# Performance work log

Hardware: AMD Instinct MI355X
Metric: run time of the kernel (lower is better)

The kernel has to match this reference:

```python
import jax, jax.numpy as jnp
import numpy as np

S, B, D, H = 197, 64, 768, 12
E, K = 8, 2
LM, LS = 2, 2
DFF = 4 * D


def layer_norm(x, s, b):
    x32 = x.astype(jnp.float32)
    mu = x32.mean(-1, keepdims=True)
    var = x32.var(-1, keepdims=True)
    y = (x32 - mu) * jax.lax.rsqrt(var + 1e-5) * s + b
    return y.astype(x.dtype)


def quick_gelu(x):
    return x * jax.nn.sigmoid(1.702 * x)


def mha(x, in_w, in_b, out_w, out_b):
    # x: [S, B, D]; torch nn.MultiheadAttention math
    s, b, d = x.shape
    hd = d // H
    qkv = x @ in_w.T + in_b  # [S, B, 3D]
    q, k, v = jnp.split(qkv, 3, axis=-1)
    def heads(t):
        return t.reshape(s, b, H, hd).transpose(1, 2, 0, 3)  # [B, H, S, hd]
    q, k, v = heads(q), heads(k), heads(v)
    scale = 1.0 / np.sqrt(hd).astype(np.float32)
    scores = jnp.einsum('bhqd,bhkd->bhqk', q * scale, k)
    attn = jax.nn.softmax(scores, axis=-1)
    o = jnp.einsum('bhqk,bhkd->bhqd', attn, v)
    o = o.transpose(2, 0, 1, 3).reshape(s, b, d)
    return o @ out_w.T + out_b


def route(flat, gate_w):
    logits = flat @ gate_w.T  # [T, E]
    probs = jax.nn.softmax(logits.astype(jnp.float32), axis=-1)
    w, idx = jax.lax.top_k(probs, K)  # [T, K]
    w = w / w.sum(-1, keepdims=True)
    w = w.astype(flat.dtype)
    # combine weights [T, E]: routing weight where expert selected, else 0
    comb = (jax.nn.one_hot(idx, E, dtype=w.dtype) * w[..., None]).sum(axis=1)
    return logits, comb


def moe_ffn(flat, comb, w1, b1, w2, b2):
    # w1: [E, DFF, D], w2: [E, D, DFF]; exact top-k math via zero combine weights
    out = jnp.zeros_like(flat)
    for e in range(E):
        h = quick_gelu(flat @ w1[e].T + b1[e])
        out = out + comb[:, e:e + 1] * (h @ w2[e].T + b2[e])
    return out


def forward(x,
            moe_ln1_s, moe_ln1_b, moe_in_w, moe_in_b, moe_out_w, moe_out_b,
            moe_ln2_s, moe_ln2_b, moe_gate_w, moe_w1, moe_b1, moe_w2, moe_b2,
            std_ln1_s, std_ln1_b, std_in_w, std_in_b, std_out_w, std_out_b,
            std_ln2_s, std_ln2_b, std_fc_w, std_fc_b, std_proj_w, std_proj_b):
    first_logits = None
    comb = None
    for i in range(LM):
        h = x + mha(layer_norm(x, moe_ln1_s[i], moe_ln1_b[i]),
                    moe_in_w[i], moe_in_b[i], moe_out_w[i], moe_out_b[i])
        hs = layer_norm(h, moe_ln2_s[i], moe_ln2_b[i])
        flat = hs.reshape(-1, D)  # [S*B, D]
        if i == 0:
            first_logits, comb = route(flat, moe_gate_w[0])
        # subsequent MoE blocks reuse the first block's routing decision
        out_flat = moe_ffn(flat, comb, moe_w1[i], moe_b1[i], moe_w2[i], moe_b2[i])
        x = h + out_flat.reshape(h.shape)
    for i in range(LS):
        x = x + mha(layer_norm(x, std_ln1_s[i], std_ln1_b[i]),
                    std_in_w[i], std_in_b[i], std_out_w[i], std_out_b[i])
        y = layer_norm(x, std_ln2_s[i], std_ln2_b[i])
        y = quick_gelu(y @ std_fc_w[i].T + std_fc_b[i])
        x = x + (y @ std_proj_w[i].T + std_proj_b[i])
    return x, first_logits


def setup_inputs() -> dict:
    key = jax.random.key(0)
    ks = jax.random.split(key, 16)
    def n(k, shape, s=0.02):
        return jax.random.normal(k, shape, jnp.float32) * s
    inp = {}
    inp['x'] = jax.random.normal(ks[0], (S, B, D), jnp.float32)
    inp['moe_ln1_s'] = jnp.ones((LM, D), jnp.float32)
    inp['moe_ln1_b'] = jnp.zeros((LM, D), jnp.float32)
    inp['moe_in_w'] = n(ks[1], (LM, 3 * D, D))
    inp['moe_in_b'] = jnp.zeros((LM, 3 * D), jnp.float32)
    inp['moe_out_w'] = n(ks[2], (LM, D, D))
    inp['moe_out_b'] = jnp.zeros((LM, D), jnp.float32)
    inp['moe_ln2_s'] = jnp.ones((LM, D), jnp.float32)
    inp['moe_ln2_b'] = jnp.zeros((LM, D), jnp.float32)
    inp['moe_gate_w'] = n(ks[3], (LM, E, D))
    inp['moe_w1'] = n(ks[4], (LM, E, DFF, D))
    inp['moe_b1'] = jnp.zeros((LM, E, DFF), jnp.float32)
    inp['moe_w2'] = n(ks[5], (LM, E, D, DFF))
    inp['moe_b2'] = jnp.zeros((LM, E, D), jnp.float32)
    inp['std_ln1_s'] = jnp.ones((LS, D), jnp.float32)
    inp['std_ln1_b'] = jnp.zeros((LS, D), jnp.float32)
    inp['std_in_w'] = n(ks[6], (LS, 3 * D, D))
    inp['std_in_b'] = jnp.zeros((LS, 3 * D), jnp.float32)
    inp['std_out_w'] = n(ks[7], (LS, D, D))
    inp['std_out_b'] = jnp.zeros((LS, D), jnp.float32)
    inp['std_ln2_s'] = jnp.ones((LS, D), jnp.float32)
    inp['std_ln2_b'] = jnp.zeros((LS, D), jnp.float32)
    inp['std_fc_w'] = n(ks[8], (LS, DFF, D))
    inp['std_fc_b'] = jnp.zeros((LS, DFF), jnp.float32)
    inp['std_proj_w'] = n(ks[9], (LS, D, DFF))
    inp['std_proj_b'] = jnp.zeros((LS, D), jnp.float32)
    return inp


def reference(x,
              moe_ln1_s, moe_ln1_b, moe_in_w, moe_in_b, moe_out_w, moe_out_b,
              moe_ln2_s, moe_ln2_b, moe_gate_w, moe_w1, moe_b1, moe_w2, moe_b2,
              std_ln1_s, std_ln1_b, std_in_w, std_in_b, std_out_w, std_out_b,
              std_ln2_s, std_ln2_b, std_fc_w, std_fc_b, std_proj_w, std_proj_b):
    return forward(x,
                   moe_ln1_s, moe_ln1_b, moe_in_w, moe_in_b, moe_out_w, moe_out_b,
                   moe_ln2_s, moe_ln2_b, moe_gate_w, moe_w1, moe_b1, moe_w2, moe_b2,
                   std_ln1_s, std_ln1_b, std_in_w, std_in_b, std_out_w, std_out_b,
                   std_ln2_s, std_ln2_b, std_fc_w, std_fc_b, std_proj_w, std_proj_b)
```

## Files before the change

### kernel.cpp

```cpp
#include <hip/hip_runtime.h>

#define TOK   12608
#define SLOTS 25216
#define DM    768
#define D3    2304
#define FF    3072
#define NH    12
#define SEQ   197
#define BAT   64
#define NE    8
#define VPAD  224

typedef short  short8  __attribute__((ext_vector_type(8)));
typedef float  floatx4 __attribute__((ext_vector_type(4)));

__device__ __forceinline__ unsigned short f2bf(float f) {
  union { float f; unsigned u; } c; c.f = f;
  unsigned r = c.u + 0x7fffu + ((c.u >> 16) & 1u);
  return (unsigned short)(r >> 16);
}
__device__ __forceinline__ float bf2f(unsigned short h) {
  union { unsigned u; float f; } c; c.u = ((unsigned)h) << 16; return c.f;
}

__device__ __forceinline__ void gl2lds16(const void* g, void* l) {
  __builtin_amdgcn_global_load_lds((const __attribute__((address_space(1))) unsigned int*)g,
                                   (__attribute__((address_space(3))) unsigned int*)l, 16, 0, 0);
}


__global__ __launch_bounds__(256) void copy_k(float* __restrict__ dst, const float* __restrict__ src, long long n4) {
  long long i = (long long)blockIdx.x * 256 + threadIdx.x;
  long long st = (long long)gridDim.x * 256;
  for (; i < n4; i += st) ((floatx4*)dst)[i] = ((const floatx4*)src)[i];
}

__global__ __launch_bounds__(256) void conv_k(unsigned short* __restrict__ dst, const float* __restrict__ src, long long n4) {
  long long i = (long long)blockIdx.x * 256 + threadIdx.x;
  long long st = (long long)gridDim.x * 256;
  for (; i < n4; i += st) {
    floatx4 v = ((const floatx4*)src)[i];
    union { unsigned short u[4]; unsigned long long ll; } o;
    o.u[0] = f2bf(v.x); o.u[1] = f2bf(v.y); o.u[2] = f2bf(v.z); o.u[3] = f2bf(v.w);
    ((unsigned long long*)dst)[i] = o.ll;
  }
}

__global__ __launch_bounds__(256) void conv2_k(unsigned short* __restrict__ dhi, unsigned short* __restrict__ dlo,
                                               const float* __restrict__ src, long long n4) {
  long long i = (long long)blockIdx.x * 256 + threadIdx.x;
  long long st = (long long)gridDim.x * 256;
  for (; i < n4; i += st) {
    floatx4 v = ((const floatx4*)src)[i];
    union { unsigned short u[4]; unsigned long long ll; } oh, ol;
    #pragma unroll
    for (int j = 0; j < 4; ++j) {
      unsigned short h = f2bf(v[j]);
      oh.u[j] = h; ol.u[j] = f2bf(v[j] - bf2f(h));
    }
    ((unsigned long long*)dhi)[i] = oh.ll;
    ((unsigned long long*)dlo)[i] = ol.ll;
  }
}

__global__ void zero_k(int* p, int n) { int i = threadIdx.x; if (i < n) p[i] = 0; }

__global__ __launch_bounds__(256) void ln_k(const float* __restrict__ x, const float* __restrict__ s,
                                            const float* __restrict__ b, unsigned short* __restrict__ out) {
  int t = blockIdx.x * 4 + (threadIdx.x >> 6);
  int lane = threadIdx.x & 63;
  const float* xr = x + (long long)t * DM;
  float v[12]; float s1 = 0.f, s2 = 0.f;
  #pragma unroll
  for (int i = 0; i < 12; ++i) { v[i] = xr[lane + i*64]; s1 += v[i]; s2 += v[i]*v[i]; }
  #pragma unroll
  for (int o = 1; o < 64; o <<= 1) { s1 += __shfl_xor(s1, o); s2 += __shfl_xor(s2, o); }
  float mu = s1 * (1.f/768.f);
  float inv = 1.f / sqrtf(s2*(1.f/768.f) - mu*mu + 1e-5f);
  unsigned short* orow = out + (long long)t * DM;
  #pragma unroll
  for (int i = 0; i < 12; ++i) { int f = lane + i*64; orow[f] = f2bf((v[i]-mu)*inv*s[f] + b[f]); }
}

__global__ __launch_bounds__(256) void ln2bf_k(const float* __restrict__ x, const float* __restrict__ s,
                                               const float* __restrict__ b, unsigned short* __restrict__ ohi,
                                               unsigned short* __restrict__ olo) {
  int t = blockIdx.x * 4 + (threadIdx.x >> 6);
  int lane = threadIdx.x & 63;
  const float* xr = x + (long long)t * DM;
  float v[12]; float s1 = 0.f, s2 = 0.f;
  #pragma unroll
  for (int i = 0; i < 12; ++i) { v[i] = xr[lane + i*64]; s1 += v[i]; s2 += v[i]*v[i]; }
  #pragma unroll
  for (int o = 1; o < 64; o <<= 1) { s1 += __shfl_xor(s1, o); s2 += __shfl_xor(s2, o); }
  float mu = s1 * (1.f/768.f);
  float inv = 1.f / sqrtf(s2*(1.f/768.f) - mu*mu + 1e-5f);
  unsigned short* rh = ohi + (long long)t * DM;
  unsigned short* rl = olo + (long long)t * DM;
  #pragma unroll
  for (int i = 0; i < 12; ++i) {
    int f = lane + i*64;
    float y = (v[i]-mu)*inv*s[f] + b[f];
    unsigned short h = f2bf(y);
    rh[f] = h; rl[f] = f2bf(y - bf2f(h));
  }
}

__global__ __launch_bounds__(256) void gate_k(const float* __restrict__ x, const float* __restrict__ s,
    const float* __restrict__ b, const float* __restrict__ gw, float* __restrict__ logitsOut,
    int* __restrict__ e0, int* __restrict__ e1, float* __restrict__ w0, float* __restrict__ w1) {
  int t = blockIdx.x * 4 + (threadIdx.x >> 6);
  int lane = threadIdx.x & 63;
  const float* xr = x + (long long)t * DM;
  float v[12]; float s1 = 0.f, s2 = 0.f;
  #pragma unroll
  for (int i = 0; i < 12; ++i) { v[i] = xr[lane + i*64]; s1 += v[i]; s2 += v[i]*v[i]; }
  #pragma unroll
  for (int o = 1; o < 64; o <<= 1) { s1 += __shfl_xor(s1, o); s2 += __shfl_xor(s2, o); }
  float mu = s1 * (1.f/768.f);
  float inv = 1.f / sqrtf(s2*(1.f/768.f) - mu*mu + 1e-5f);
  float lg[8];
  #pragma unroll
  for (int e = 0; e < 8; ++e) lg[e] = 0.f;
  #pragma unroll
  for (int i = 0; i < 12; ++i) {
    int f = lane + i*64;
    float y = (v[i]-mu)*inv*s[f] + b[f];
    #pragma unroll
    for (int e = 0; e < 8; ++e) lg[e] += y * gw[e*DM + f];
  }
  #pragma unroll
  for (int e = 0; e < 8; ++e) {
    #pragma unroll
    for (int o = 1; o < 64; o <<= 1) lg[e] += __shfl_xor(lg[e], o);
  }
  if (lane == 0) {
    int a0 = 0;
    #pragma unroll
    for (int e = 1; e < 8; ++e) if (lg[e] > lg[a0]) a0 = e;
    int a1 = (a0 == 0) ? 1 : 0;
    #pragma unroll
    for (int e = 0; e < 8; ++e) if (e != a0 && lg[e] > lg[a1]) a1 = e;
    float mx = lg[a0];
    float pa = __expf(lg[a0]-mx), pb = __expf(lg[a1]-mx), iw = 1.f/(pa+pb);
    e0[t] = a0; e1[t] = a1; w0[t] = pa*iw; w1[t] = pb*iw;
    #pragma unroll
    for (int e = 0; e < 8; ++e) logitsOut[(long long)t*8 + e] = lg[e];
  }
}

__global__ __launch_bounds__(256) void hist_k(const int* __restrict__ e0, const int* __restrict__ e1,
                                              int* __restrict__ counts) {
  __shared__ int hc[8];
  int tid = threadIdx.x;
  if (tid < 8) hc[tid] = 0;
  __syncthreads();
  int c[8];
  #pragma unroll
  for (int e = 0; e < 8; ++e) c[e] = 0;
  for (int t = blockIdx.x * 256 + tid; t < TOK; t += gridDim.x * 256) {
    int a = e0[t], b = e1[t];
    #pragma unroll
    for (int e = 0; e < 8; ++e) c[e] += (a == e) + (b == e);
  }
  #pragma unroll
  for (int e = 0; e < 8; ++e) {
    #pragma unroll
    for (int o = 1; o < 64; o <<= 1) c[e] += __shfl_xor(c[e], o);
  }
  if ((tid & 63) == 0) {
    #pragma unroll
    for (int e = 0; e < 8; ++e) atomicAdd(&hc[e], c[e]);
  }
  __syncthreads();
  if (tid < 8 && hc[tid]) atomicAdd(&counts[tid], hc[tid]);
}

__global__ void tilemap_k(const int* __restrict__ counts, int* __restrict__ cur,
                          int4* __restrict__ tileMap, int* __restrict__ tileCount) {
  if (threadIdx.x == 0 && blockIdx.x == 0) {
    int off = 0, nt = 0;
    for (int e = 0; e < 8; ++e) {
      cur[e] = off;
      int cnt = counts[e];
      for (int s = 0; s < cnt; s += 128) {
        int rows = cnt - s; if (rows > 128) rows = 128;
        tileMap[nt++] = make_int4(e, off + s, rows, 0);
      }
      off += cnt;
    }
    *tileCount = nt;
  }
}

__global__ __launch_bounds__(256) void scatter_k(const int* __restrict__ e0, const int* __restrict__ e1,
    const float* __restrict__ w0, const float* __restrict__ w1, int* __restrict__ cur,
    int* __restrict__ perm, float* __restrict__ wslot, int* __restrict__ slotA, int* __restrict__ slotB) {
  int t = blockIdx.x * 256 + threadIdx.x;
  int lane = threadIdx.x & 63;
  bool valid = t < TOK;
  int a = valid ? e0[t] : -1;
  int b = valid ? e1[t] : -1;
  int sa = 0, sb = 0;
  #pragma unroll
  for (int e = 0; e < 8; ++e) {
    unsigned long long m = __ballot(a == e);
    int cnt = (int)__popcll(m);
    int base = 0;
    if (lane == 0 && cnt) base = atomicAdd(&cur[e], cnt);
    base = __shfl(base, 0);
    if (a == e) sa = base + (int)__popcll(m & ((1ull << lane) - 1ull));

    unsigned long long m2 = __ballot(b == e);
    int cnt2 = (int)__popcll(m2);
    int base2 = 0;
    if (lane == 0 && cnt2) base2 = atomicAdd(&cur[e], cnt2);
    base2 = __shfl(base2, 0);
    if (b == e) sb = base2 + (int)__popcll(m2 & ((1ull << lane) - 1ull));
  }
  if (valid) {
    perm[sa] = t; wslot[sa] = w0[t]; slotA[t] = sa;
    perm[sb] = t; wslot[sb] = w1[t]; slotB[t] = sb;
  }
}

__global__ __launch_bounds__(256) void combine_k(float* __restrict__ x, const float* __restrict__ Y,
    const int* __restrict__ sA, const int* __restrict__ sB) {
  int idx = blockIdx.x * 256 + threadIdx.x;
  int t = idx / (DM/4), f = idx % (DM/4);
  const floatx4* ya = (const floatx4*)(Y + (long long)sA[t]*DM);
  const floatx4* yb = (const floatx4*)(Y + (long long)sB[t]*DM);
  floatx4* xp = (floatx4*)(x + (long long)t*DM);
  xp[f] = xp[f] + ya[f] + yb[f];
}

__global__ __launch_bounds__(256) void vtrans_k(const unsigned short* __restrict__ hi,
    const unsigned short* __restrict__ lo, unsigned short* __restrict__ vThi,
    unsigned short* __restrict__ vTlo) {
  __shared__ unsigned short tH[64][65], tL[64][65];
  int bh = blockIdx.x; int b = bh / NH, h = bh % NH;
  int t = threadIdx.x; int d = t & 63, sl = t >> 6;
  for (int chunk = 0; chunk < 4; ++chunk) {
    __syncthreads();
    #pragma unroll
    for (int r = 0; r < 16; ++r) {
      int sp = r*4 + sl;
      int sg = chunk*64 + sp;
      unsigned short vh = 0, vl = 0;
      if (sg < SEQ) {
        long long off = (long long)(sg*BAT + b)*D3 + 2*DM + h*64 + d;
        vh = hi[off]; vl = lo[off];
      }
      tH[sp][d] = vh; tL[sp][d] = vl;
    }
    __syncthreads();
    int s2 = t & 63, dd0 = t >> 6;
    if (chunk*64 + s2 < VPAD) {
      #pragma unroll
      for (int r = 0; r < 16; ++r) {
        int dd = r*4 + dd0;
        long long oi = ((long long)bh*64 + dd)*VPAD + chunk*64 + s2;
        vThi[oi] = tH[s2][dd];
        vTlo[oi] = tL[s2][dd];
      }
    }
  }
}

template<int MODE, bool GATHER, bool PERM>
__global__ __launch_bounds__(256) void gemm_k(
    const unsigned short* __restrict__ A, const unsigned short* __restrict__ Bw,
    const float* __restrict__ bias, int M, int N, int K,
    const int* __restrict__ perm, const int4* __restrict__ tileMap,
    const int* __restrict__ tileCount, const float* __restrict__ wslot,
    unsigned short* __restrict__ outB, float* __restrict__ outF,
    long long bStrideE, int biasStrideE) {
  int e = 0, rowStart, rows;
  if (GATHER) {
    if ((int)blockIdx.y >= *tileCount) return;
    int4 tm = tileMap[blockIdx.y];
    e = tm.x; rowStart = tm.y; rows = tm.z;
  } else {
    rowStart = blockIdx.y * 128;
    rows = M - rowStart; if (rows > 128) rows = 128;
  }
  __shared__ __align__(16) unsigned short As[2][128*32];
  __shared__ __align__(16) unsigned short Bs[2][128*32];
  int tid = threadIdx.x, lane = tid & 63, w = tid >> 6;
  int n0 = blockIdx.x * 128;
  const unsigned short* Bp = Bw + (long long)e * bStrideE;
  const float* biasp = bias + (long long)e * biasStrideE;

  const char* aSrc[2]; const char* bSrc[2];
  unsigned short* ldsA[2][2]; unsigned short* ldsB[2][2];
  #pragma unroll
  for (int j = 0; j < 2; ++j) {
    int row = j*64 + w*16 + (lane >> 2);
    int kb  = (lane & 3) * 16;
    int ar  = row < rows ? row : rows - 1;
    long long srcRow;
    if (GATHER) { int slot = rowStart + ar; srcRow = PERM ? (long long)perm[slot] : (long long)slot; }
    else        srcRow = rowStart + ar;
    aSrc[j] = (const char*)(A + srcRow * (long long)K) + kb;
    bSrc[j] = (const char*)(Bp + (long long)(n0 + row) * K) + kb;
    #pragma unroll
    for (int p = 0; p < 2; ++p) {
      ldsA[p][j] = &As[p][j*2048 + w*512];
      ldsB[p][j] = &Bs[p][j*2048 + w*512];
    }
  }

  floatx4 acc[4][4];
  floatx4 zf = {0.f, 0.f, 0.f, 0.f};
  #pragma unroll
  for (int i = 0; i < 4; ++i)
    #pragma unroll
    for (int j = 0; j < 4; ++j) acc[i][j] = zf;

  int wm = w >> 1, wn = w & 1;
  int aOff = (wm*64 + (lane & 15))*32 + (lane >> 4)*8;
  int bOff = (wn*64 + (lane & 15))*32 + (lane >> 4)*8;

  for (int k0 = 0; k0 < K; k0 += 64) {
    long long kb2 = (long long)k0 * 2;
    #pragma unroll
    for (int p = 0; p < 2; ++p)
      #pragma unroll
      for (int j = 0; j < 2; ++j) {
        gl2lds16(aSrc[j] + kb2 + p*64, ldsA[p][j]);
        gl2lds16(bSrc[j] + kb2 + p*64, ldsB[p][j]);
      }
    __syncthreads();
    #pragma unroll
    for (int p = 0; p < 2; ++p) {
      short8 aF[4], bF[4];
      #pragma unroll
      for (int i = 0; i < 4; ++i) aF[i] = *(const short8*)&As[p][aOff + i*512];
      #pragma unroll
      for (int j = 0; j < 4; ++j) bF[j] = *(const short8*)&Bs[p][bOff + j*512];
      #pragma unroll
      for (int i = 0; i < 4; ++i)
        #pragma unroll
        for (int j = 0; j < 4; ++j)
          acc[i][j] = __builtin_amdgcn_mfma_f32_16x16x32_bf16(aF[i], bF[j], acc[i][j], 0, 0, 0);
    }
    __syncthreads();
  }

  int quad = lane >> 4, c = lane & 15;
  #pragma unroll
  for (int i = 0; i < 4; ++i) {
    int rl0 = wm*64 + i*16 + quad*4;
    #pragma unroll
    for (int j = 0; j < 4; ++j) {
      int col = n0 + wn*64 + j*16 + c;
      float bc = biasp[col];
      #pragma unroll
      for (int r = 0; r < 4; ++r) {
        int rl = rl0 + r;
        if (rl < rows) {
          long long orow = (long long)(rowStart + rl);
          float v = acc[i][j][r] + bc;
          if (MODE == 0) {
            outB[orow*N + col] = f2bf(v);
          } else if (MODE == 1) {
            float g = v / (1.f + __expf(-1.702f * v));
            outB[orow*N + col] = f2bf(g);
          } else if (MODE == 2) {
            outF[orow*N + col] += v;
          } else {
            outF[orow*N + col] = wslot[orow] * v;
          }
        }
      }
    }
  }
}

template<int HPMODE>
__global__ __launch_bounds__(256) void gemm_hp_k(
    const unsigned short* __restrict__ Ahi, const unsigned short* __restrict__ Alo,
    const unsigned short* __restrict__ Bhi, const unsigned short* __restrict__ Blo,
    const float* __restrict__ bias, int M, int N, int K,
    unsigned short* __restrict__ oHi, unsigned short* __restrict__ oLo,
    float* __restrict__ outF) {
  int rowStart = blockIdx.y * 128;
  int rows = M - rowStart; if (rows > 128) rows = 128;
  __shared__ __align__(16) unsigned short AsH[128*32];
  __shared__ __align__(16) unsigned short AsL[128*32];
  __shared__ __align__(16) unsigned short BsH[128*32];
  __shared__ __align__(16) unsigned short BsL[128*32];
  int tid = threadIdx.x, lane = tid & 63, w = tid >> 6;
  int n0 = blockIdx.x * 128;

  const char *aH[2], *aL[2], *bH[2], *bL[2];
  unsigned short *lAH[2], *lAL[2], *lBH[2], *lBL[2];
  #pragma unroll
  for (int j = 0; j < 2; ++j) {
    int row = j*64 + w*16 + (lane >> 2);
    int kb  = (lane & 3) * 16;
    int ar  = row < rows ? row : rows - 1;
    long long srcRow = rowStart + ar;
    aH[j] = (const char*)(Ahi + srcRow * (long long)K) + kb;
    aL[j] = (const char*)(Alo + srcRow * (long long)K) + kb;
    bH[j] = (const char*)(Bhi + (long long)(n0 + row) * K) + kb;
    bL[j] = (const char*)(Blo + (long long)(n0 + row) * K) + kb;
    lAH[j] = &AsH[j*2048 + w*512]; lAL[j] = &AsL[j*2048 + w*512];
    lBH[j] = &BsH[j*2048 + w*512]; lBL[j] = &BsL[j*2048 + w*512];
  }

  floatx4 acc[4][4];
  floatx4 zf = {0.f, 0.f, 0.f, 0.f};
  #pragma unroll
  for (int i = 0; i < 4; ++i)
    #pragma unroll
    for (int j = 0; j < 4; ++j) acc[i][j] = zf;

  int wm = w >> 1, wn = w & 1;
  int aOff = (wm*64 + (lane & 15))*32 + (lane >> 4)*8;
  int bOff = (wn*64 + (lane & 15))*32 + (lane >> 4)*8;

  for (int k0 = 0; k0 < K; k0 += 32) {
    long long kb2 = (long long)k0 * 2;
    #pragma unroll
    for (int j = 0; j < 2; ++j) {
      gl2lds16(aH[j] + kb2, lAH[j]);
      gl2lds16(aL[j] + kb2, lAL[j]);
      gl2lds16(bH[j] + kb2, lBH[j]);
      gl2lds16(bL[j] + kb2, lBL[j]);
    }
    __syncthreads();
    short8 ah[4], al[4], bh[4], bl[4];
    #pragma unroll
    for (int i = 0; i < 4; ++i) {
      ah[i] = *(const short8*)&AsH[aOff + i*512];
      al[i] = *(const short8*)&AsL[aOff + i*512];
    }
    #pragma unroll
    for (int j = 0; j < 4; ++j) {
      bh[j] = *(const short8*)&BsH[bOff + j*512];
      bl[j] = *(const short8*)&BsL[bOff + j*512];
    }
    #pragma unroll
    for (int i = 0; i < 4; ++i)
      #pragma unroll
      for (int j = 0; j < 4; ++j) {
        acc[i][j] = __builtin_amdgcn_mfma_f32_16x16x32_bf16(ah[i], bh[j], acc[i][j], 0, 0, 0);
        acc[i][j] = __builtin_amdgcn_mfma_f32_16x16x32_bf16(ah[i], bl[j], acc[i][j], 0, 0, 0);
        acc[i][j] = __builtin_amdgcn_mfma_f32_16x16x32_bf16(al[i], bh[j], acc[i][j], 0, 0, 0);
        acc[i][j] = __builtin_amdgcn_mfma_f32_16x16x32_bf16(al[i], bl[j], acc[i][j], 0, 0, 0);
      }
    __syncthreads();
  }

  int quad = lane >> 4, c = lane & 15;
  #pragma unroll
  for (int i = 0; i < 4; ++i) {
    int rl0 = wm*64 + i*16 + quad*4;
    #pragma unroll
    for (int j = 0; j < 4; ++j) {
      int col = n0 + wn*64 + j*16 + c;
      float bc = bias[col];
      #pragma unroll
      for (int r = 0; r < 4; ++r) {
        int rl = rl0 + r;
        if (rl < rows) {
          long long orow = (long long)(rowStart + rl);
          float v = acc[i][j][r] + bc;
          if (HPMODE == 0) {
            unsigned short h = f2bf(v);
            oHi[orow*N + col] = h;
            oLo[orow*N + col] = f2bf(v - bf2f(h));
          } else {
            outF[orow*N + col] += v;
          }
        }
      }
    }
  }
}

__global__ __launch_bounds__(256) void attn_k(const unsigned short* __restrict__ qkv,
                                              unsigned short* __restrict__ out) {
  __shared__ __align__(16) unsigned short Vt[64*224];
  __shared__ __align__(16) unsigned short Pb[4][16*224];
  int bh = blockIdx.x; int b = bh / NH, h = bh % NH;
  int tid = threadIdx.x, lane = tid & 63, w = tid >> 6;
  for (int idx = tid; idx < 224*64; idx += 256) {
    int key = idx >> 6, d = idx & 63;
    unsigned short v = 0;
    if (key < SEQ) v = qkv[(long long)(key*BAT + b)*D3 + 2*DM + h*64 + d];
    Vt[d*224 + key] = v;
  }
  for (int idx = tid; idx < 4*16*224; idx += 256) ((unsigned short*)Pb)[idx] = 0;
  __syncthreads();

  int quad = lane >> 4, c = lane & 15;
  for (int qt = w; qt < 13; qt += 4) {
    int q0 = qt * 16;
    int qrow = q0 + c; int sq = qrow < SEQ ? qrow : SEQ-1;
    const unsigned short* qp = qkv + (long long)(sq*BAT + b)*D3 + h*64 + quad*8;
    short8 aq0 = *(const short8*)qp;
    short8 aq1 = *(const short8*)(qp + 32);
    floatx4 sc[13];
    #pragma unroll
    for (int nt = 0; nt < 13; ++nt) {
      int key = nt*16 + c; int sk = key < SEQ ? key : SEQ-1;
      const unsigned short* kp = qkv + (long long)(sk*BAT + b)*D3 + DM + h*64 + quad*8;
      short8 bk0 = *(const short8*)kp;
      short8 bk1 = *(const short8*)(kp + 32);
      floatx4 z = {0.f,0.f,0.f,0.f};
      z = __builtin_amdgcn_mfma_f32_16x16x32_bf16(aq0, bk0, z, 0, 0, 0);
      z = __builtin_amdgcn_mfma_f32_16x16x32_bf16(aq1, bk1, z, 0, 0, 0);
      sc[nt] = z;
    }
    float mx[4], sm[4];
    #pragma unroll
    for (int r = 0; r < 4; ++r) mx[r] = -1e30f;
    #pragma unroll
    for (int nt = 0; nt < 13; ++nt) {
      bool ok = (nt*16 + c) < SEQ;
      #pragma unroll
      for (int r = 0; r < 4; ++r) {
        float v = ok ? sc[nt][r] * 0.125f : -1e30f;
        sc[nt][r] = v;
        mx[r] = fmaxf(mx[r], v);
      }
    }
    #pragma unroll
    for (int r = 0; r < 4; ++r) {
      #pragma unroll
      for (int o = 1; o < 16; o <<= 1) mx[r] = fmaxf(mx[r], __shfl_xor(mx[r], o));
      sm[r] = 0.f;
    }
    #pragma unroll
    for (int nt = 0; nt < 13; ++nt) {
      #pragma unroll
      for (int r = 0; r < 4; ++r) { float p = __expf(sc[nt][r] - mx[r]); sc[nt][r] = p; sm[r] += p; }
    }
    #pragma unroll
    for (int r = 0; r < 4; ++r) {
      #pragma unroll
      for (int o = 1; o < 16; o <<= 1) sm[r] += __shfl_xor(sm[r], o);
      sm[r] = 1.f / sm[r];
    }
    #pragma unroll
    for (int nt = 0; nt < 13; ++nt) {
      #pragma unroll
      for (int r = 0; r < 4; ++r)
        Pb[w][(quad*4 + r)*224 + nt*16 + c] = f2bf(sc[nt][r] * sm[r]);
    }
    #pragma unroll
    for (int n2 = 0; n2 < 4; ++n2) {
      floatx4 o4 = {0.f,0.f,0.f,0.f};
      #pragma unroll
      for (int ks = 0; ks < 7; ++ks) {
        short8 ap = *(const short8*)&Pb[w][c*224 + ks*32 + quad*8];
        short8 bv = *(const short8*)&Vt[(n2*16 + c)*224 + ks*32 + quad*8];
        o4 = __builtin_amdgcn_mfma_f32_16x16x32_bf16(ap, bv, o4, 0, 0, 0);
      }
      #pragma unroll
      for (int r = 0; r < 4; ++r) {
        int qg = q0 + quad*4 + r;
        if (qg < SEQ)
          out[(long long)(qg*BAT + b)*DM + h*64 + n2*16 + c] = f2bf(o4[r]);
      }
    }
  }
}

__global__ __launch_bounds__(256) void attn_hp_k(
    const unsigned short* __restrict__ qh, const unsigned short* __restrict__ ql,
    const unsigned short* __restrict__ vThi, const unsigned short* __restrict__ vTlo,
    unsigned short* __restrict__ oHi, unsigned short* __restrict__ oLo) {
  __shared__ __align__(16) unsigned short PbH[4][16*224];
  __shared__ __align__(16) unsigned short PbL[4][16*224];
  int bh = blockIdx.x; int b = bh / NH, h = bh % NH;
  int tid = threadIdx.x, lane = tid & 63, w = tid >> 6;
  for (int idx = lane; idx < 16*224; idx += 64) { PbH[w][idx] = 0; PbL[w][idx] = 0; }

  int quad = lane >> 4, c = lane & 15;
  const unsigned short* vHb = vThi + (long long)bh * 64 * VPAD;
  const unsigned short* vLb = vTlo + (long long)bh * 64 * VPAD;

  for (int qt = w; qt < 13; qt += 4) {
    int q0 = qt * 16;
    int qrow = q0 + c; int sq = qrow < SEQ ? qrow : SEQ-1;
    long long qoff = (long long)(sq*BAT + b)*D3 + h*64 + quad*8;
    short8 qh0 = *(const short8*)(qh + qoff);
    short8 qh1 = *(const short8*)(qh + qoff + 32);
    short8 ql0 = *(const short8*)(ql + qoff);
    short8 ql1 = *(const short8*)(ql + qoff + 32);
    floatx4 sc[13];
    #pragma unroll
    for (int nt = 0; nt < 13; ++nt) {
      int key = nt*16 + c; int sk = key < SEQ ? key : SEQ-1;
      long long koff = (long long)(sk*BAT + b)*D3 + DM + h*64 + quad*8;
      short8 kh0 = *(const short8*)(qh + koff);
      short8 kh1 = *(const short8*)(qh + koff + 32);
      short8 kl0 = *(const short8*)(ql + koff);
      short8 kl1 = *(const short8*)(ql + koff + 32);
      floatx4 z = {0.f,0.f,0.f,0.f};
      z = __builtin_amdgcn_mfma_f32_16x16x32_bf16(qh0, kh0, z, 0, 0, 0);
      z = __builtin_amdgcn_mfma_f32_16x16x32_bf16(qh0, kl0, z, 0, 0, 0);
      z = __builtin_amdgcn_mfma_f32_16x16x32_bf16(ql0, kh0, z, 0, 0, 0);
      z = __builtin_amdgcn_mfma_f32_16x16x32_bf16(ql0, kl0, z, 0, 0, 0);
      z = __builtin_amdgcn_mfma_f32_16x16x32_bf16(qh1, kh1, z, 0, 0, 0);
      z = __builtin_amdgcn_mfma_f32_16x16x32_bf16(qh1, kl1, z, 0, 0, 0);
      z = __builtin_amdgcn_mfma_f32_16x16x32_bf16(ql1, kh1, z, 0, 0, 0);
      z = __builtin_amdgcn_mfma_f32_16x16x32_bf16(ql1, kl1, z, 0, 0, 0);
      sc[nt] = z;
    }
    float mx[4], sm[4];
    #pragma unroll
    for (int r = 0; r < 4; ++r) mx[r] = -1e30f;
    #pragma unroll
    for (int nt = 0; nt < 13; ++nt) {
      bool ok = (nt*16 + c) < SEQ;
      #pragma unroll
      for (int r = 0; r < 4; ++r) {
        float v = ok ? sc[nt][r] * 0.125f : -1e30f;
        sc[nt][r] = v;
        mx[r] = fmaxf(mx[r], v);
      }
    }
    #pragma unroll
    for (int r = 0; r < 4; ++r) {
      #pragma unroll
      for (int o = 1; o < 16; o <<= 1) mx[r] = fmaxf(mx[r], __shfl_xor(mx[r], o));
      sm[r] = 0.f;
    }
    #pragma unroll
    for (int nt = 0; nt < 13; ++nt) {
      #pragma unroll
      for (int r = 0; r < 4; ++r) { float p = __expf(sc[nt][r] - mx[r]); sc[nt][r] = p; sm[r] += p; }
    }
    #pragma unroll
    for (int r = 0; r < 4; ++r) {
      #pragma unroll
      for (int o = 1; o < 16; o <<= 1) sm[r] += __shfl_xor(sm[r], o);
      sm[r] = 1.f / sm[r];
    }
    #pragma unroll
    for (int nt = 0; nt < 13; ++nt) {
      #pragma unroll
      for (int r = 0; r < 4; ++r) {
        float p = sc[nt][r] * sm[r];
        unsigned short ph = f2bf(p);
        PbH[w][(quad*4 + r)*224 + nt*16 + c] = ph;
        PbL[w][(quad*4 + r)*224 + nt*16 + c] = f2bf(p - bf2f(ph));
      }
    }
    #pragma unroll
    for (int n2 = 0; n2 < 4; ++n2) {
      floatx4 o4 = {0.f,0.f,0.f,0.f};
      const unsigned short* vh = vHb + (long long)(n2*16 + c)*VPAD;
      const unsigned short* vl = vLb + (long long)(n2*16 + c)*VPAD;
      #pragma unroll
      for (int ks = 0; ks < 7; ++ks) {
        short8 ph = *(const short8*)&PbH[w][c*224 + ks*32 + quad*8];
        short8 pl = *(const short8*)&PbL[w][c*224 + ks*32 + quad*8];
        short8 bvh = *(const short8*)(vh + ks*32 + quad*8);
        short8 bvl = *(const short8*)(vl + ks*32 + quad*8);
        o4 = __builtin_amdgcn_mfma_f32_16x16x32_bf16(ph, bvh, o4, 0, 0, 0);
        o4 = __builtin_amdgcn_mfma_f32_16x16x32_bf16(ph, bvl, o4, 0, 0, 0);
        o4 = __builtin_amdgcn_mfma_f32_16x16x32_bf16(pl, bvh, o4, 0, 0, 0);
        o4 = __builtin_amdgcn_mfma_f32_16x16x32_bf16(pl, bvl, o4, 0, 0, 0);
      }
      #pragma unroll
      for (int r = 0; r < 4; ++r) {
        int qg = q0 + quad*4 + r;
        if (qg < SEQ) {
          long long oi = (long long)(qg*BAT + b)*DM + h*64 + n2*16 + c;
          float v = o4[r];
          unsigned short hh = f2bf(v);
          oHi[oi] = hh;
          oLo[oi] = f2bf(v - bf2f(hh));
        }
      }
    }
  }
}


extern "C" void kernel_launch(void* const* d_in, const int* in_sizes, int n_in,
                              void* d_out, int out_size, void* d_ws, size_t ws_size,
                              hipStream_t stream) {
  const float* in_x    = (const float*)d_in[0];
  const float* p_mln1s = (const float*)d_in[1];
  const float* p_mln1b = (const float*)d_in[2];
  const float* p_minw  = (const float*)d_in[3];
  const float* p_minb  = (const float*)d_in[4];
  const float* p_moutw = (const float*)d_in[5];
  const float* p_moutb = (const float*)d_in[6];
  const float* p_mln2s = (const float*)d_in[7];
  const float* p_mln2b = (const float*)d_in[8];
  const float* p_gate  = (const float*)d_in[9];
  const float* p_w1    = (const float*)d_in[10];
  const float* p_b1    = (const float*)d_in[11];
  const float* p_w2    = (const float*)d_in[12];
  const float* p_b2    = (const float*)d_in[13];
  const float* p_sln1s = (const float*)d_in[14];
  const float* p_sln1b = (const float*)d_in[15];
  const float* p_sinw  = (const float*)d_in[16];
  const float* p_sinb  = (const float*)d_in[17];
  const float* p_soutw = (const float*)d_in[18];
  const float* p_soutb = (const float*)d_in[19];
  const float* p_sln2s = (const float*)d_in[20];
  const float* p_sln2b = (const float*)d_in[21];
  const float* p_sfcw  = (const float*)d_in[22];
  const float* p_sfcb  = (const float*)d_in[23];
  const float* p_sprojw= (const float*)d_in[24];
  const float* p_sprojb= (const float*)d_in[25];

  float* xout   = (float*)d_out;
  float* logits = xout + (long long)TOK * DM;

  char* wp = (char*)d_ws;
  auto carve = [&](long long bytes) -> char* {
    char* r = wp; wp += (bytes + 255) & ~255LL; return r;
  };
  unsigned short* lnB   = (unsigned short*)carve((long long)TOK * DM * 2);
  unsigned short* lnLo  = (unsigned short*)carve((long long)TOK * DM * 2);
  unsigned short* bigB  = (unsigned short*)carve((long long)SLOTS * FF * 2);
  unsigned short* attnB = (unsigned short*)carve((long long)TOK * DM * 2);
  unsigned short* attnLo= (unsigned short*)carve((long long)TOK * DM * 2);
  float*          Ybuf  = (float*)carve((long long)SLOTS * DM * 4);
  unsigned short* vThi  = (unsigned short*)carve((long long)BAT*NH*64*VPAD*2 + 64);
  unsigned short* vTlo  = (unsigned short*)carve((long long)BAT*NH*64*VPAD*2 + 64);
  unsigned short* wreg  = (unsigned short*)carve(40108032LL * 2);
  unsigned short* wInLo = (unsigned short*)carve((long long)D3*DM*2);
  unsigned short* wOutLo= (unsigned short*)carve((long long)DM*DM*2);
  int*   counts   = (int*)carve(64);
  int*   cur      = (int*)carve(64);
  int*   tileCnt  = (int*)carve(64);
  int4*  tileMap  = (int4*)carve(256 * 16);
  int*   e0 = (int*)carve(TOK*4); int* e1 = (int*)carve(TOK*4);
  float* w0 = (float*)carve(TOK*4); float* w1 = (float*)carve(TOK*4);
  int*   perm  = (int*)carve(SLOTS*4);
  float* wslot = (float*)carve(SLOTS*4);
  int*   slotA = (int*)carve(TOK*4); int* slotB = (int*)carve(TOK*4);
  (void)in_sizes; (void)n_in; (void)out_size; (void)ws_size;

  unsigned short* qkvB  = bigB;
  unsigned short* qkvLo = (unsigned short*)Ybuf;
  unsigned short* Hbuf  = bigB;
  unsigned short* wIn  = wreg;
  unsigned short* wOut = wreg + 1769472;
  unsigned short* wFc1 = wreg + 2359296;
  unsigned short* wFc2 = wreg + 21233664;

  copy_k<<<4096, 256, 0, stream>>>(xout, in_x, (long long)TOK*DM/4);

  for (int layer = 0; layer < 4; ++layer) {
    bool moe = layer < 2;
    bool hp  = (layer == 0);
    int li = moe ? layer : layer - 2;
    const float* ln1s = moe ? p_mln1s + li*DM : p_sln1s + li*DM;
    const float* ln1b = moe ? p_mln1b + li*DM : p_sln1b + li*DM;
    const float* inw  = moe ? p_minw + (long long)li*D3*DM : p_sinw + (long long)li*D3*DM;
    const float* inb  = moe ? p_minb + li*D3 : p_sinb + li*D3;
    const float* outw = moe ? p_moutw + (long long)li*DM*DM : p_soutw + (long long)li*DM*DM;
    const float* outb = moe ? p_moutb + li*DM : p_soutb + li*DM;
    const float* ln2s = moe ? p_mln2s + li*DM : p_sln2s + li*DM;
    const float* ln2b = moe ? p_mln2b + li*DM : p_sln2b + li*DM;

    if (hp) {
      conv2_k<<<2048, 256, 0, stream>>>(wIn, wInLo, inw, (long long)D3*DM/4);
      conv2_k<<<1024, 256, 0, stream>>>(wOut, wOutLo, outw, (long long)DM*DM/4);
    } else {
      conv_k<<<2048, 256, 0, stream>>>(wIn,  inw,  (long long)D3*DM/4);
      conv_k<<<1024, 256, 0, stream>>>(wOut, outw, (long long)DM*DM/4);
    }
    if (moe) {
      conv_k<<<4096, 256, 0, stream>>>(wFc1, p_w1 + (long long)li*NE*FF*DM, (long long)NE*FF*DM/4);
      conv_k<<<4096, 256, 0, stream>>>(wFc2, p_w2 + (long long)li*NE*DM*FF, (long long)NE*DM*FF/4);
    } else {
      conv_k<<<2048, 256, 0, stream>>>(wFc1, p_sfcw   + (long long)li*FF*DM, (long long)FF*DM/4);
      conv_k<<<2048, 256, 0, stream>>>(wFc2, p_sprojw + (long long)li*DM*FF, (long long)DM*FF/4);
    }

    if (hp) {
      ln2bf_k<<<TOK/4, 256, 0, stream>>>(xout, ln1s, ln1b, lnB, lnLo);
      gemm_hp_k<0><<<dim3(D3/128, 99), 256, 0, stream>>>(lnB, lnLo, wIn, wInLo, inb,
          TOK, D3, DM, qkvB, qkvLo, nullptr);
      vtrans_k<<<BAT*NH, 256, 0, stream>>>(qkvB, qkvLo, vThi, vTlo);
      attn_hp_k<<<BAT*NH, 256, 0, stream>>>(qkvB, qkvLo, vThi, vTlo, attnB, attnLo);
      gemm_hp_k<1><<<dim3(DM/128, 99), 256, 0, stream>>>(attnB, attnLo, wOut, wOutLo, outb,
          TOK, DM, DM, nullptr, nullptr, xout);
    } else {
      ln_k<<<TOK/4, 256, 0, stream>>>(xout, ln1s, ln1b, lnB);
      gemm_k<0,false,false><<<dim3(D3/128, 99), 256, 0, stream>>>(lnB, wIn, inb, TOK, D3, DM,
          nullptr, nullptr, nullptr, nullptr, qkvB, nullptr, 0, 0);
      attn_k<<<BAT*NH, 256, 0, stream>>>(qkvB, attnB);
      gemm_k<2,false,false><<<dim3(DM/128, 99), 256, 0, stream>>>(attnB, wOut, outb, TOK, DM, DM,
          nullptr, nullptr, nullptr, nullptr, nullptr, xout, 0, 0);
    }
    ln_k<<<TOK/4, 256, 0, stream>>>(xout, ln2s, ln2b, lnB);

    if (layer == 0) {
      zero_k<<<1, 64, 0, stream>>>(counts, 8);
      gate_k<<<TOK/4, 256, 0, stream>>>(xout, ln2s, ln2b, p_gate, logits, e0, e1, w0, w1);
      hist_k<<<64, 256, 0, stream>>>(e0, e1, counts);
      tilemap_k<<<1, 1, 0, stream>>>(counts, cur, tileMap, tileCnt);
      scatter_k<<<(TOK+255)/256, 256, 0, stream>>>(e0, e1, w0, w1, cur, perm, wslot, slotA, slotB);
    }

    if (moe) {
      gemm_k<1,true,true><<<dim3(FF/128, 205), 256, 0, stream>>>(lnB, wFc1, p_b1 + (long long)li*NE*FF,
          SLOTS, FF, DM, perm, tileMap, tileCnt, nullptr, Hbuf, nullptr, (long long)FF*DM, FF);
      gemm_k<3,true,false><<<dim3(DM/128, 205), 256, 0, stream>>>(Hbuf, wFc2, p_b2 + (long long)li*NE*DM,
          SLOTS, DM, FF, nullptr, tileMap, tileCnt, wslot, nullptr, Ybuf, (long long)DM*FF, DM);
      combine_k<<<TOK*(DM/4)/256, 256, 0, stream>>>(xout, Ybuf, slotA, slotB);
    } else {
      gemm_k<1,false,false><<<dim3(FF/128, 99), 256, 0, stream>>>(lnB, wFc1, p_sfcb + li*FF,
          TOK, FF, DM, nullptr, nullptr, nullptr, nullptr, Hbuf, nullptr, 0, 0);
      gemm_k<2,false,false><<<dim3(DM/128, 99), 256, 0, stream>>>(Hbuf, wFc2, p_sprojb + li*DM,
          TOK, DM, FF, nullptr, nullptr, nullptr, nullptr, nullptr, xout, 0, 0);
    }
  }
}
```

Measured before the change: 3.039 ms.

## Add 256x256-tile GEMM kernel with 4-stage LDS pipeline for wide-N GEMMs

```diff
diff --git a/kernel.cpp b/kernel.cpp
--- a/kernel.cpp
+++ b/kernel.cpp
@@ -177,9 +177,10 @@
 }
 
 __global__ void tilemap_k(const int* __restrict__ counts, int* __restrict__ cur,
-                          int4* __restrict__ tileMap, int* __restrict__ tileCount) {
+                          int4* __restrict__ tileMap, int* __restrict__ tileCount,
+                          int4* __restrict__ tileMap2, int* __restrict__ tileCount2) {
   if (threadIdx.x == 0 && blockIdx.x == 0) {
-    int off = 0, nt = 0;
+    int off = 0, nt = 0, n2 = 0;
     for (int e = 0; e < 8; ++e) {
       cur[e] = off;
       int cnt = counts[e];
@@ -187,9 +188,14 @@
         int rows = cnt - s; if (rows > 128) rows = 128;
         tileMap[nt++] = make_int4(e, off + s, rows, 0);
       }
+      for (int s = 0; s < cnt; s += 256) {
+        int rows = cnt - s; if (rows > 256) rows = 256;
+        tileMap2[n2++] = make_int4(e, off + s, rows, 0);
+      }
       off += cnt;
     }
     *tileCount = nt;
+    *tileCount2 = n2;
   }
 }
 
@@ -361,6 +367,144 @@
         if (rl < rows) {
           long long orow = (long long)(rowStart + rl);
           float v = acc[i][j][r] + bc;
+          if (MODE == 0) {
+            outB[orow*N + col] = f2bf(v);
+          } else if (MODE == 1) {
+            float g = v / (1.f + __expf(-1.702f * v));
+            outB[orow*N + col] = f2bf(g);
+          } else if (MODE == 2) {
+            outF[orow*N + col] += v;
+          } else {
+            outF[orow*N + col] = wslot[orow] * v;
+          }
+        }
+      }
+    }
+  }
+}
+
+template<int MODE, bool GATHER, bool PERM>
+__global__ __launch_bounds__(512, 2) void gemm2_k(
+    const unsigned short* __restrict__ A, const unsigned short* __restrict__ Bw,
+    const float* __restrict__ bias, int M, int N, int K,
+    const int* __restrict__ perm, const int4* __restrict__ tileMap,
+    const int* __restrict__ tileCount, const float* __restrict__ wslot,
+    unsigned short* __restrict__ outB, float* __restrict__ outF,
+    long long bStrideE, int biasStrideE) {
+  int e = 0, rowStart, rows;
+  if (GATHER) {
+    if ((int)blockIdx.y >= *tileCount) return;
+    int4 tm = tileMap[blockIdx.y];
+    e = tm.x; rowStart = tm.y; rows = tm.z;
+  } else {
+    rowStart = blockIdx.y * 256;
+    rows = M - rowStart; if (rows > 256) rows = 256;
+  }
+  __shared__ __align__(16) unsigned short smem[65536];
+  int tid = threadIdx.x, lane = tid & 63, w = tid >> 6;
+  int wm = w >> 2, wn = w & 3;
+  int n0 = blockIdx.x * 256;
+  const unsigned short* Bp = Bw + (long long)e * bStrideE;
+  const float* biasp = bias + (long long)e * biasStrideE;
+  const int nkt = K >> 5;
+
+  int sRowL = w*16 + (lane >> 2);
+  int sSlot = (lane & 3) ^ ((lane >> 3) & 3);
+  long long srcA0, srcA1;
+  {
+    int r0 = sRowL, r1 = sRowL + 128;
+    int ar0 = r0 < rows ? r0 : rows - 1;
+    int ar1 = r1 < rows ? r1 : rows - 1;
+    if (GATHER) {
+      srcA0 = PERM ? (long long)perm[rowStart + ar0] : (long long)(rowStart + ar0);
+      srcA1 = PERM ? (long long)perm[rowStart + ar1] : (long long)(rowStart + ar1);
+    } else { srcA0 = rowStart + ar0; srcA1 = rowStart + ar1; }
+  }
+  const char* aP0 = (const char*)(A + srcA0 * (long long)K) + sSlot*16;
+  const char* aP1 = (const char*)(A + srcA1 * (long long)K) + sSlot*16;
+  const char* bP0 = (const char*)(Bp + (long long)(n0 + sRowL) * K) + sSlot*16;
+  const char* bP1 = (const char*)(Bp + (long long)(n0 + sRowL + 128) * K) + sSlot*16;
+
+  auto stA = [&](int tt) {
+    unsigned short* l = &smem[(tt & 3)*16384 + w*512];
+    long long ko = (long long)tt * 64;
+    gl2lds16(aP0 + ko, l);
+    gl2lds16(aP1 + ko, l + 4096);
+  };
+  auto stB = [&](int tt) {
+    unsigned short* l = &smem[(tt & 3)*16384 + 8192 + w*512];
+    long long ko = (long long)tt * 64;
+    gl2lds16(bP0 + ko, l);
+    gl2lds16(bP1 + ko, l + 4096);
+  };
+
+  int laneR = lane & 15, kq = lane >> 4;
+  int sx = kq ^ ((laneR >> 1) & 3);
+  int aRd = (wm*128 + laneR)*32 + sx*8;
+  int bRd = (wn*64  + laneR)*32 + sx*8;
+
+  floatx4 acc[8][4];
+  floatx4 zf = {0.f, 0.f, 0.f, 0.f};
+  #pragma unroll
+  for (int i = 0; i < 8; ++i)
+    #pragma unroll
+    for (int j = 0; j < 4; ++j) acc[i][j] = zf;
+
+  for (int tt = 0; tt < 3 && tt < nkt; ++tt) { stA(tt); stB(tt); }
+  if (nkt > 2)      { asm volatile("s_waitcnt vmcnt(8)" ::: "memory"); }
+  else if (nkt > 1) { asm volatile("s_waitcnt vmcnt(4)" ::: "memory"); }
+  else              { asm volatile("s_waitcnt vmcnt(0)" ::: "memory"); }
+  __builtin_amdgcn_s_barrier();
+
+  for (int t = 0; t < nkt; ++t) {
+    const int buf = (t & 3) * 16384;
+    short8 aF[4], bF[4];
+    #pragma unroll
+    for (int cf = 0; cf < 4; ++cf) bF[cf] = *(const short8*)&smem[buf + 8192 + bRd + cf*512];
+    #pragma unroll
+    for (int rf = 0; rf < 4; ++rf) aF[rf] = *(const short8*)&smem[buf + aRd + rf*512];
+    if (t + 3 < nkt) stA(t + 3);
+    asm volatile("s_waitcnt lgkmcnt(0)" ::: "memory");
+    __builtin_amdgcn_sched_barrier(0);
+    __builtin_amdgcn_s_setprio(1);
+    #pragma unroll
+    for (int rf = 0; rf < 4; ++rf)
+      #pragma unroll
+      for (int cf = 0; cf < 4; ++cf)
+        acc[rf][cf] = __builtin_amdgcn_mfma_f32_16x16x32_bf16(aF[rf], bF[cf], acc[rf][cf], 0, 0, 0);
+    __builtin_amdgcn_s_setprio(0);
+    __builtin_amdgcn_s_barrier();
+    #pragma unroll
+    for (int rf = 0; rf < 4; ++rf) aF[rf] = *(const short8*)&smem[buf + aRd + (rf+4)*512];
+    if (t + 3 < nkt) stB(t + 3);
+    asm volatile("s_waitcnt lgkmcnt(0)" ::: "memory");
+    __builtin_amdgcn_sched_barrier(0);
+    __builtin_amdgcn_s_setprio(1);
+    #pragma unroll
+    for (int rf = 0; rf < 4; ++rf)
+      #pragma unroll
+      for (int cf = 0; cf < 4; ++cf)
+        acc[rf+4][cf] = __builtin_amdgcn_mfma_f32_16x16x32_bf16(aF[rf], bF[cf], acc[rf+4][cf], 0, 0, 0);
+    __builtin_amdgcn_s_setprio(0);
+    if (t + 3 < nkt)      { asm volatile("s_waitcnt vmcnt(8)" ::: "memory"); }
+    else if (t + 2 < nkt) { asm volatile("s_waitcnt vmcnt(4)" ::: "memory"); }
+    else if (t + 1 < nkt) { asm volatile("s_waitcnt vmcnt(0)" ::: "memory"); }
+    if (t + 1 < nkt) __builtin_amdgcn_s_barrier();
+  }
+
+  #pragma unroll
+  for (int rf = 0; rf < 8; ++rf) {
+    int rl0 = wm*128 + rf*16 + kq*4;
+    #pragma unroll
+    for (int cf = 0; cf < 4; ++cf) {
+      int col = n0 + wn*64 + cf*16 + laneR;
+      float bc = biasp[col];
+      #pragma unroll
+      for (int r = 0; r < 4; ++r) {
+        int rl = rl0 + r;
+        if (rl < rows) {
+          long long orow = (long long)(rowStart + rl);
+          float v = acc[rf][cf][r] + bc;
           if (MODE == 0) {
             outB[orow*N + col] = f2bf(v);
           } else if (MODE == 1) {
@@ -735,6 +879,8 @@
   int*   cur      = (int*)carve(64);
   int*   tileCnt  = (int*)carve(64);
   int4*  tileMap  = (int4*)carve(256 * 16);
+  int*   tileCnt2 = (int*)carve(64);
+  int4*  tileMap2 = (int4*)carve(256 * 16);
   int*   e0 = (int*)carve(TOK*4); int* e1 = (int*)carve(TOK*4);
   float* w0 = (float*)carve(TOK*4); float* w1 = (float*)carve(TOK*4);
   int*   perm  = (int*)carve(SLOTS*4);
@@ -790,7 +936,7 @@
           TOK, DM, DM, nullptr, nullptr, xout);
     } else {
       ln_k<<<TOK/4, 256, 0, stream>>>(xout, ln1s, ln1b, lnB);
-      gemm_k<0,false,false><<<dim3(D3/128, 99), 256, 0, stream>>>(lnB, wIn, inb, TOK, D3, DM,
+      gemm2_k<0,false,false><<<dim3(D3/256, 50), 512, 0, stream>>>(lnB, wIn, inb, TOK, D3, DM,
           nullptr, nullptr, nullptr, nullptr, qkvB, nullptr, 0, 0);
       attn_k<<<BAT*NH, 256, 0, stream>>>(qkvB, attnB);
       gemm_k<2,false,false><<<dim3(DM/128, 99), 256, 0, stream>>>(attnB, wOut, outb, TOK, DM, DM,
@@ -802,18 +948,18 @@
       zero_k<<<1, 64, 0, stream>>>(counts, 8);
       gate_k<<<TOK/4, 256, 0, stream>>>(xout, ln2s, ln2b, p_gate, logits, e0, e1, w0, w1);
       hist_k<<<64, 256, 0, stream>>>(e0, e1, counts);
-      tilemap_k<<<1, 1, 0, stream>>>(counts, cur, tileMap, tileCnt);
+      tilemap_k<<<1, 1, 0, stream>>>(counts, cur, tileMap, tileCnt, tileMap2, tileCnt2);
       scatter_k<<<(TOK+255)/256, 256, 0, stream>>>(e0, e1, w0, w1, cur, perm, wslot, slotA, slotB);
     }
 
     if (moe) {
-      gemm_k<1,true,true><<<dim3(FF/128, 205), 256, 0, stream>>>(lnB, wFc1, p_b1 + (long long)li*NE*FF,
-          SLOTS, FF, DM, perm, tileMap, tileCnt, nullptr, Hbuf, nullptr, (long long)FF*DM, FF);
+      gemm2_k<1,true,true><<<dim3(FF/256, 106), 512, 0, stream>>>(lnB, wFc1, p_b1 + (long long)li*NE*FF,
+          SLOTS, FF, DM, perm, tileMap2, tileCnt2, nullptr, Hbuf, nullptr, (long long)FF*DM, FF);
       gemm_k<3,true,false><<<dim3(DM/128, 205), 256, 0, stream>>>(Hbuf, wFc2, p_b2 + (long long)li*NE*DM,
           SLOTS, DM, FF, nullptr, tileMap, tileCnt, wslot, nullptr, Ybuf, (long long)DM*FF, DM);
       combine_k<<<TOK*(DM/4)/256, 256, 0, stream>>>(xout, Ybuf, slotA, slotB);
     } else {
-      gemm_k<1,false,false><<<dim3(FF/128, 99), 256, 0, stream>>>(lnB, wFc1, p_sfcb + li*FF,
+      gemm2_k<1,false,false><<<dim3(FF/256, 50), 512, 0, stream>>>(lnB, wFc1, p_sfcb + li*FF,
           TOK, FF, DM, nullptr, nullptr, nullptr, nullptr, Hbuf, nullptr, 0, 0);
       gemm_k<2,false,false><<<dim3(DM/128, 99), 256, 0, stream>>>(Hbuf, wFc2, p_sprojb + li*DM,
           TOK, DM, FF, nullptr, nullptr, nullptr, nullptr, nullptr, xout, 0, 0);
```

After: 3.418 ms. 1.12x slower.

## Drop lo*lo split-bf16 MFMA terms and vectorize GEMM epilogue stores via transposed MFMA

Applied to the files above, without the earlier changes.

```diff
diff --git a/kernel.cpp b/kernel.cpp
--- a/kernel.cpp
+++ b/kernel.cpp
@@ -342,35 +342,46 @@
       for (int i = 0; i < 4; ++i)
         #pragma unroll
         for (int j = 0; j < 4; ++j)
-          acc[i][j] = __builtin_amdgcn_mfma_f32_16x16x32_bf16(aF[i], bF[j], acc[i][j], 0, 0, 0);
+          acc[i][j] = __builtin_amdgcn_mfma_f32_16x16x32_bf16(bF[j], aF[i], acc[i][j], 0, 0, 0);
     }
     __syncthreads();
   }
 
-  int quad = lane >> 4, c = lane & 15;
+  int c = lane & 15, quad = lane >> 4;
   #pragma unroll
   for (int i = 0; i < 4; ++i) {
-    int rl0 = wm*64 + i*16 + quad*4;
-    #pragma unroll
-    for (int j = 0; j < 4; ++j) {
-      int col = n0 + wn*64 + j*16 + c;
-      float bc = biasp[col];
-      #pragma unroll
-      for (int r = 0; r < 4; ++r) {
-        int rl = rl0 + r;
-        if (rl < rows) {
-          long long orow = (long long)(rowStart + rl);
-          float v = acc[i][j][r] + bc;
-          if (MODE == 0) {
-            outB[orow*N + col] = f2bf(v);
-          } else if (MODE == 1) {
-            float g = v / (1.f + __expf(-1.702f * v));
-            outB[orow*N + col] = f2bf(g);
-          } else if (MODE == 2) {
-            outF[orow*N + col] += v;
-          } else {
-            outF[orow*N + col] = wslot[orow] * v;
+    int rl = wm*64 + i*16 + c;
+    if (rl < rows) {
+      long long orow = (long long)(rowStart + rl);
+      float ws = (MODE == 3) ? wslot[orow] : 0.f;
+      #pragma unroll
+      for (int j = 0; j < 4; ++j) {
+        int col = n0 + wn*64 + j*16 + quad*4;
+        floatx4 bc4 = *(const floatx4*)&biasp[col];
+        floatx4 v4;
+        #pragma unroll
+        for (int r = 0; r < 4; ++r) v4[r] = acc[i][j][r] + bc4[r];
+        if (MODE == 0) {
+          union { unsigned short u[4]; unsigned long long ll; } o;
+          #pragma unroll
+          for (int r = 0; r < 4; ++r) o.u[r] = f2bf(v4[r]);
+          *(unsigned long long*)&outB[orow*N + col] = o.ll;
+        } else if (MODE == 1) {
+          union { unsigned short u[4]; unsigned long long ll; } o;
+          #pragma unroll
+          for (int r = 0; r < 4; ++r) {
+            float g = v4[r] / (1.f + __expf(-1.702f * v4[r]));
+            o.u[r] = f2bf(g);
           }
+          *(unsigned long long*)&outB[orow*N + col] = o.ll;
+        } else if (MODE == 2) {
+          floatx4* op = (floatx4*)&outF[orow*N + col];
+          *op = *op + v4;
+        } else {
+          floatx4 sv;
+          #pragma unroll
+          for (int r = 0; r < 4; ++r) sv[r] = ws * v4[r];
+          *(floatx4*)&outF[orow*N + col] = sv;
         }
       }
     }
@@ -445,35 +456,38 @@
     for (int i = 0; i < 4; ++i)
       #pragma unroll
       for (int j = 0; j < 4; ++j) {
-        acc[i][j] = __builtin_amdgcn_mfma_f32_16x16x32_bf16(ah[i], bh[j], acc[i][j], 0, 0, 0);
-        acc[i][j] = __builtin_amdgcn_mfma_f32_16x16x32_bf16(ah[i], bl[j], acc[i][j], 0, 0, 0);
-        acc[i][j] = __builtin_amdgcn_mfma_f32_16x16x32_bf16(al[i], bh[j], acc[i][j], 0, 0, 0);
-        acc[i][j] = __builtin_amdgcn_mfma_f32_16x16x32_bf16(al[i], bl[j], acc[i][j], 0, 0, 0);
+        acc[i][j] = __builtin_amdgcn_mfma_f32_16x16x32_bf16(bh[j], ah[i], acc[i][j], 0, 0, 0);
+        acc[i][j] = __builtin_amdgcn_mfma_f32_16x16x32_bf16(bl[j], ah[i], acc[i][j], 0, 0, 0);
+        acc[i][j] = __builtin_amdgcn_mfma_f32_16x16x32_bf16(bh[j], al[i], acc[i][j], 0, 0, 0);
       }
     __syncthreads();
   }
 
-  int quad = lane >> 4, c = lane & 15;
+  int c = lane & 15, quad = lane >> 4;
   #pragma unroll
   for (int i = 0; i < 4; ++i) {
-    int rl0 = wm*64 + i*16 + quad*4;
-    #pragma unroll
-    for (int j = 0; j < 4; ++j) {
-      int col = n0 + wn*64 + j*16 + c;
-      float bc = bias[col];
-      #pragma unroll
-      for (int r = 0; r < 4; ++r) {
-        int rl = rl0 + r;
-        if (rl < rows) {
-          long long orow = (long long)(rowStart + rl);
-          float v = acc[i][j][r] + bc;
-          if (HPMODE == 0) {
-            unsigned short h = f2bf(v);
-            oHi[orow*N + col] = h;
-            oLo[orow*N + col] = f2bf(v - bf2f(h));
-          } else {
-            outF[orow*N + col] += v;
+    int rl = wm*64 + i*16 + c;
+    if (rl < rows) {
+      long long orow = (long long)(rowStart + rl);
+      #pragma unroll
+      for (int j = 0; j < 4; ++j) {
+        int col = n0 + wn*64 + j*16 + quad*4;
+        floatx4 bc4 = *(const floatx4*)&bias[col];
+        floatx4 v4;
+        #pragma unroll
+        for (int r = 0; r < 4; ++r) v4[r] = acc[i][j][r] + bc4[r];
+        if (HPMODE == 0) {
+          union { unsigned short u[4]; unsigned long long ll; } oh, ol;
+          #pragma unroll
+          for (int r = 0; r < 4; ++r) {
+            unsigned short h = f2bf(v4[r]);
+            oh.u[r] = h; ol.u[r] = f2bf(v4[r] - bf2f(h));
           }
+          *(unsigned long long*)&oHi[orow*N + col] = oh.ll;
+          *(unsigned long long*)&oLo[orow*N + col] = ol.ll;
+        } else {
+          floatx4* op = (floatx4*)&outF[orow*N + col];
+          *op = *op + v4;
         }
       }
     }
@@ -604,11 +618,9 @@
       z = __builtin_amdgcn_mfma_f32_16x16x32_bf16(qh0, kh0, z, 0, 0, 0);
       z = __builtin_amdgcn_mfma_f32_16x16x32_bf16(qh0, kl0, z, 0, 0, 0);
       z = __builtin_amdgcn_mfma_f32_16x16x32_bf16(ql0, kh0, z, 0, 0, 0);
-      z = __builtin_amdgcn_mfma_f32_16x16x32_bf16(ql0, kl0, z, 0, 0, 0);
       z = __builtin_amdgcn_mfma_f32_16x16x32_bf16(qh1, kh1, z, 0, 0, 0);
       z = __builtin_amdgcn_mfma_f32_16x16x32_bf16(qh1, kl1, z, 0, 0, 0);
       z = __builtin_amdgcn_mfma_f32_16x16x32_bf16(ql1, kh1, z, 0, 0, 0);
-      z = __builtin_amdgcn_mfma_f32_16x16x32_bf16(ql1, kl1, z, 0, 0, 0);
       sc[nt] = z;
     }
     float mx[4], sm[4];
@@ -665,7 +677,6 @@
         o4 = __builtin_amdgcn_mfma_f32_16x16x32_bf16(ph, bvh, o4, 0, 0, 0);
         o4 = __builtin_amdgcn_mfma_f32_16x16x32_bf16(ph, bvl, o4, 0, 0, 0);
         o4 = __builtin_amdgcn_mfma_f32_16x16x32_bf16(pl, bvh, o4, 0, 0, 0);
-        o4 = __builtin_amdgcn_mfma_f32_16x16x32_bf16(pl, bvl, o4, 0, 0, 0);
       }
       #pragma unroll
       for (int r = 0; r < 4; ++r) {
```

Result: slower. 3.126 ms (+2.9%).
